# Optimization experiments

Hardware: AMD Instinct MI355X
Metric: run time of the kernel (lower is better)

## Reference

```python
import jax, jax.numpy as jnp
import numpy as np

N_NODES = 20000
N_EDGES = 320000
N_RELS = 200
DESC_LEN = 16
DIM_G = 64
DIM_WORD = 300
DIM_HIDDEN = 256
H_DIR = DIM_HIDDEN // 2  # per-direction GRU hidden
N_CLASS = 2000
V_WORD = 30000
V_DESC = 30000
B, T = 4, 32


def setup_inputs() -> dict:
    key = jax.random.key(0)
    ks = jax.random.split(key, 24)
    inp = {}
    # index tensors (pad token is 0; generate tokens in [1, V) so all positions valid)
    inp['questions'] = jax.random.randint(ks[0], (B, T), 1, V_WORD)
    inp['node_descs'] = jax.random.randint(ks[1], (N_NODES, DESC_LEN), 1, V_DESC)
    inp['edge_src'] = jax.random.randint(ks[2], (N_EDGES,), 0, N_NODES)
    inp['edge_dst'] = jax.random.randint(ks[3], (N_EDGES,), 0, N_NODES)
    inp['edge_type'] = jax.random.randint(ks[4], (N_EDGES,), 0, N_RELS)
    # embeddings (normal with std 1/sqrt(dim) as in original init)
    inp['emb_word'] = jax.random.normal(ks[5], (V_WORD, DIM_WORD)) / np.sqrt(DIM_WORD)
    inp['emb_desc'] = jax.random.normal(ks[6], (V_DESC, DIM_G)) / np.sqrt(DIM_G)
    # BiGRU params (gates order r,z,n; concatenated along last dim)
    s = 0.1
    inp['Wx_f'] = jax.random.normal(ks[7], (DIM_WORD, 3 * H_DIR)) * s
    inp['Wh_f'] = jax.random.normal(ks[8], (H_DIR, 3 * H_DIR)) * s
    inp['bx_f'] = jnp.zeros((3 * H_DIR,))
    inp['bh_f'] = jnp.zeros((3 * H_DIR,))
    inp['Wx_b'] = jax.random.normal(ks[9], (DIM_WORD, 3 * H_DIR)) * s
    inp['Wh_b'] = jax.random.normal(ks[10], (H_DIR, 3 * H_DIR)) * s
    inp['bx_b'] = jnp.zeros((3 * H_DIR,))
    inp['bh_b'] = jnp.zeros((3 * H_DIR,))
    # lin_h_to_g (kaiming-ish scale)
    inp['W_hg'] = jax.random.normal(ks[11], (DIM_HIDDEN, DIM_G)) * np.sqrt(2.0 / DIM_HIDDEN)
    inp['b_hg'] = jnp.zeros((DIM_G,))
    # RGCN basis decomposition
    inp['bases'] = jax.random.normal(ks[12], (1, DIM_G, DIM_G)) * np.sqrt(1.0 / DIM_G)
    inp['w_comp'] = jax.random.normal(ks[13], (N_RELS, 1))
    inp['rgcn_bias'] = jnp.zeros((DIM_G,))
    # classifier
    inp['W1'] = jax.random.normal(ks[14], (DIM_G + DIM_HIDDEN, 1024)) * np.sqrt(2.0 / (DIM_G + DIM_HIDDEN))
    inp['b1'] = jnp.zeros((1024,))
    inp['W2'] = jax.random.normal(ks[15], (1024, N_CLASS)) * np.sqrt(2.0 / 1024)
    inp['b2'] = jnp.zeros((N_CLASS,))
    return inp


def _gru_last_hidden(x, mask, Wx, Wh, bx, bh):
    """Run a GRU over time; hidden only updates where mask is True.
    x: [B,T,D], mask: [B,T]. Returns final hidden [B,H]."""
    bsz = x.shape[0]
    h0 = jnp.zeros((bsz, Wh.shape[0]), x.dtype)
    gx_all = x @ Wx + bx  # [B,T,3H] precompute input gates

    def step(h, inputs):
        gx, mt = inputs  # [B,3H], [B]
        gh = h @ Wh + bh
        xr, xz, xn = jnp.split(gx, 3, axis=-1)
        hr, hz, hn = jnp.split(gh, 3, axis=-1)
        r = jax.nn.sigmoid(xr + hr)
        z = jax.nn.sigmoid(xz + hz)
        n = jnp.tanh(xn + r * hn)
        h_new = (1.0 - z) * n + z * h
        h = jnp.where(mt[:, None], h_new, h)
        return h, None

    hT, _ = jax.lax.scan(step, h0, (gx_all.transpose(1, 0, 2), mask.T))
    return hT


def _rel_graph_conv(h, edge_src, edge_dst, edge_type, bases, w_comp, bias):
    """Basis-decomposed RGCN layer (DGL RelGraphConv, norm=None, no self-loop).
    h: [B,N,G]. W_r = sum_k w_comp[r,k] * bases[k]."""
    n = h.shape[1]
    # project through each basis first: [B,N,K,O]
    hb = jnp.einsum('bng,kgo->bnko', h, bases)
    # per-edge message: gather src, combine with relation coefficients -> [B,E,O]
    msg = jnp.einsum('beko,ek->beo', hb[:, edge_src], w_comp[edge_type])
    # scatter-add to destination nodes
    agg = jax.vmap(lambda m: jax.ops.segment_sum(m, edge_dst, num_segments=n))(msg)
    return jax.nn.relu(agg + bias)


def reference(questions, node_descs, edge_src, edge_dst, edge_type,
              emb_word, emb_desc,
              Wx_f, Wh_f, bx_f, bh_f, Wx_b, Wh_b, bx_b, bh_b,
              W_hg, b_hg, bases, w_comp, rgcn_bias,
              W1, b1, W2, b2):
    # ---- question encoding (BiGRU over non-pad tokens; pad id = 0) ----
    mask = questions != 0  # [B,T]
    x = emb_word[questions]  # [B,T,Dw] (dropout is identity at eval)
    hf = _gru_last_hidden(x, mask, Wx_f, Wh_f, bx_f, bh_f)
    hb = _gru_last_hidden(x[:, ::-1], mask[:, ::-1], Wx_b, Wh_b, bx_b, bh_b)
    q_emb = jnp.concatenate([hf, hb], axis=-1)  # [B, dim_hidden]

    # ---- attention-weighted node features from descriptions ----
    desc_emb = emb_desc[node_descs]          # [N,L,G]
    q_g = q_emb @ W_hg + b_hg                # [B,G]
    attn1 = jax.nn.softmax(jnp.einsum('nlg,bg->bnl', desc_emb, q_g), axis=-1)
    node_feat = jnp.einsum('bnl,nlg->bng', attn1, desc_emb)  # [B,N,G]

    # ---- one RGCN hidden layer over the KB graph ----
    node_feat = _rel_graph_conv(node_feat, edge_src, edge_dst, edge_type,
                                bases, w_comp, rgcn_bias)

    # ---- attention pooling over nodes ----
    attn2 = jax.nn.softmax(jnp.einsum('bng,bg->bn', node_feat, q_g), axis=1)
    node_agg = jnp.einsum('bn,bng->bg', attn2, node_feat)    # [B,G]

    # ---- classifier ----
    feat = jnp.concatenate([node_agg, q_emb], axis=-1)       # [B, G+H]
    logits = jax.nn.relu(feat @ W1 + b1) @ W2 + b2           # [B, n_class]
    return logits
```

## Files before the change

### kernel.cpp

```cpp
#include <hip/hip_runtime.h>
#include <hip/hip_bf16.h>
#include <math.h>

typedef __hip_bfloat16 bf16;

#define NNODES 20000
#define NEDGES 320000
#define DLEN   16
#define G      64
#define DW     300
#define DH     256
#define HD     128
#define G3     384
#define NCLS   2000
#define NB     4
#define TT     32
#define A2BLK  1024
#define A2MID  64

#define NBLK_CVT  384
#define NBLK_GX2  1536
#define NBLK_HIST ((NEDGES + 255) / 256)
#define NBLK_SCAT ((NEDGES + 255) / 256)

__device__ __forceinline__ float ld(const float* p, size_t i) { return p[i]; }
__device__ __forceinline__ float ld(const bf16* p, size_t i) { return __bfloat162float(p[i]); }
__device__ __forceinline__ void st(float* p, size_t i, float v) { p[i] = v; }
__device__ __forceinline__ void st(bf16* p, size_t i, float v) { p[i] = __float2bfloat16(v); }
__device__ __forceinline__ float relu(float x) { return (x < 0.f) ? 0.f : x; }

struct __align__(8) bf4 { bf16 x, y, z, w; };

#define OFF_FLAG  ((size_t)0)
#define OFF_GX    (OFF_FLAG + 4)
#define OFF_WHF   (OFF_GX   + 2*NB*TT*G3)
#define OFF_QEMB  (OFF_WHF  + 2*HD*G3)
#define OFF_QG    (OFF_QEMB + NB*DH)
#define OFF_NF    (OFF_QG   + NB*G)
#define OFF_HB    (OFF_NF   + (size_t)NB*NNODES*G)
#define OFF_PART  (OFF_HB   + (size_t)NB*NNODES*G)
#define OFF_PART2 (OFF_PART + (size_t)A2BLK*NB*66)
#define OFF_DEG   (OFF_PART2+ (size_t)A2MID*NB*66)
#define OFF_OFFS  (OFF_DEG  + NNODES)
#define OFF_RANK  (OFF_OFFS + NNODES + 8)
#define OFF_EPACK (OFF_RANK + NEDGES)
#define OFF_HID   (OFF_EPACK + 2*(size_t)NEDGES)

__global__ void k_init(const unsigned* probe, int* flag, int* deg) {
    int i = blockIdx.x * 256 + threadIdx.x;
    if (i < NNODES) deg[i] = 0;
    if (blockIdx.x == 0 && threadIdx.x < 64) {
        int cnt = 0;
        for (int k = threadIdx.x; k < 4096; k += 64) {
            unsigned lo = probe[k] & 0xFFFFu;
            unsigned e = (lo >> 7) & 0xFFu;
            cnt += (e >= 0x66u && e <= 0x7Eu) ? 1 : 0;
        }
#pragma unroll
        for (int off = 1; off < 64; off <<= 1) cnt += __shfl_xor(cnt, off, 64);
        if (threadIdx.x == 0) *flag = (2 * cnt > 4096) ? 1 : 0;
    }
}

template <typename T>
__device__ void cvt_body(int id, const void* Whf_, const void* Whb_, float* whf) {
    if (id >= 2 * HD * G3) return;
    int d = id / (HD * G3), r = id % (HD * G3);
    const T* W = (const T*)(d ? Whb_ : Whf_);
    whf[id] = ld(W, (size_t)r);
}

template <typename T>
__device__ void gx2_body(int bx2, const int* questions, const void* emb_word_,
                         const void* Wxf_, const void* bxf_,
                         const void* Wxb_, const void* bxb_, float* gx,
                         float* xs, float* psum) {
    int tid = threadIdx.x;
    int jt = bx2 % 6;
    int rid = bx2 / 6;
    int step = rid & 31;
    int b = (rid >> 5) & 3;
    int d = rid >> 7;
    int t = d ? (TT - 1 - step) : step;
    int tok = questions[b * TT + t];
    const T* row = (const T*)emb_word_ + (size_t)tok * DW;
    for (int k = tid; k < DW; k += 256) xs[k] = ld(row, (size_t)k);
    __syncthreads();
    int lane = tid & 63, phase = tid >> 6;
    int j = jt * 64 + lane;
    const T* Wx = (const T*)(d ? Wxb_ : Wxf_);
    float acc = 0.f;
    int k0 = phase * 75;
#pragma unroll 15
    for (int kk = 0; kk < 75; kk++) {
        int k = k0 + kk;
        acc += xs[k] * ld(Wx, (size_t)k * G3 + j);
    }
    psum[tid] = acc;
    __syncthreads();
    if (phase == 0) {
        const T* bx = (const T*)(d ? bxb_ : bxf_);
        float tot = ld(bx, (size_t)j)
                  + psum[lane] + psum[64 + lane] + psum[128 + lane] + psum[192 + lane];
        gx[(size_t)rid * G3 + j] = tot;
    }
}

__global__ void k_prep(const int* flag, const void* Whf, const void* Whb, float* whf,
                       const int* questions, const void* emb_word,
                       const void* Wxf, const void* bxf,
                       const void* Wxb, const void* bxb, float* gx,
                       const int* edge_dst, int* deg, int* rank) {
    __shared__ float xs[DW];
    __shared__ float psum[256];
    int bx = blockIdx.x;
    int tid = threadIdx.x;
    if (bx < NBLK_CVT) {
        int id = bx * 256 + tid;
        if (*flag) cvt_body<bf16>(id, Whf, Whb, whf);
        else       cvt_body<float>(id, Whf, Whb, whf);
    } else if (bx < NBLK_CVT + NBLK_GX2) {
        int bx2 = bx - NBLK_CVT;
        if (*flag) gx2_body<bf16>(bx2, questions, emb_word, Wxf, bxf, Wxb, bxb, gx, xs, psum);
        else       gx2_body<float>(bx2, questions, emb_word, Wxf, bxf, Wxb, bxb, gx, xs, psum);
    } else {
        int e = (bx - NBLK_CVT - NBLK_GX2) * 256 + tid;
        if (e < NEDGES) rank[e] = atomicAdd(&deg[edge_dst[e]], 1);
    }
}

template <typename T>
__device__ void gru_body(const int* questions, const float* gx, const float* whf,
                         const void* bhf_, const void* bhb_, float* qemb,
                         float* hsm, float* ghs) {
    int tid = threadIdx.x;
    int d = blockIdx.x >> 2, b = blockIdx.x & 3;
    int half = tid / G3, j = tid - half * G3;
    const float* wh = whf + (size_t)d * HD * G3 + (size_t)half * 64 * G3 + j;
    float w[64];
#pragma unroll
    for (int m = 0; m < 64; m++) w[m] = wh[(size_t)m * G3];
    const T* bh = (const T*)(d ? bhb_ : bhf_);
    float bhj = (half == 0) ? ld(bh, (size_t)j) : 0.f;
    if (tid < HD) hsm[tid] = 0.f;
    const float* gxb = gx + ((size_t)(d * NB + b)) * TT * G3;
    __syncthreads();
    const float4* h4 = (const float4*)(hsm + half * 64);
    for (int step = 0; step < TT; step++) {
        float acc = bhj;
#pragma unroll
        for (int m4 = 0; m4 < 16; m4++) {
            float4 hp = h4[m4];
            acc = fmaf(hp.x, w[4 * m4 + 0], acc);
            acc = fmaf(hp.y, w[4 * m4 + 1], acc);
            acc = fmaf(hp.z, w[4 * m4 + 2], acc);
            acc = fmaf(hp.w, w[4 * m4 + 3], acc);
        }
        ghs[half * G3 + j] = acc;
        __syncthreads();
        if (tid < HD) {
            const float* gxp = gxb + step * G3;
            int t = d ? (TT - 1 - step) : step;
            bool msk = questions[b * TT + t] != 0;
            float gr = ghs[tid] + ghs[G3 + tid];
            float gz = ghs[HD + tid] + ghs[G3 + HD + tid];
            float gn = ghs[2 * HD + tid] + ghs[G3 + 2 * HD + tid];
            float r = 1.f / (1.f + expf(-(gxp[tid] + gr)));
            float z = 1.f / (1.f + expf(-(gxp[HD + tid] + gz)));
            float n = tanhf(gxp[2 * HD + tid] + r * gn);
            float hn = (1.f - z) * n + z * hsm[tid];
            if (msk) hsm[tid] = hn;
        }
        __syncthreads();
    }
    if (tid < HD) qemb[b * DH + d * HD + tid] = hsm[tid];
}

__device__ void scan_body(const int* deg, int* offs, int* wtot) {
    int t = threadIdx.x;
    int lane = t & 63, wave = t >> 6;
    int c[27];
    int base = t * 27;
    int run = 0;
#pragma unroll
    for (int i = 0; i < 27; i++) {
        int v = (base + i < NNODES) ? deg[base + i] : 0;
        c[i] = run;
        run += v;
    }
    int myrun = run, inc = run;
#pragma unroll
    for (int off = 1; off < 64; off <<= 1) {
        int u = __shfl_up(inc, off, 64);
        if (lane >= off) inc += u;
    }
    if (lane == 63) wtot[wave] = inc;
    __syncthreads();
    if (t == 0) {
        int s = 0;
#pragma unroll
        for (int i = 0; i < 12; i++) { int v = wtot[i]; wtot[i] = s; s += v; }
        offs[NNODES] = s;
    }
    __syncthreads();
    int ebase = wtot[wave] + inc - myrun;
#pragma unroll
    for (int i = 0; i < 27; i++) {
        if (base + i < NNODES) offs[base + i] = ebase + c[i];
    }
}

__global__ __launch_bounds__(2 * G3) void k_gru(const int* flag, const int* questions,
                                                const float* gx, const float* whf,
                                                const void* bhf, const void* bhb, float* qemb,
                                                const int* deg, int* offs) {
    __shared__ __align__(16) float hsm[HD];
    __shared__ float ghs[2 * G3];
    __shared__ int wtot[12];
    if (blockIdx.x < 8) {
        if (*flag) gru_body<bf16>(questions, gx, whf, bhf, bhb, qemb, hsm, ghs);
        else       gru_body<float>(questions, gx, whf, bhf, bhb, qemb, hsm, ghs);
    } else {
        scan_body(deg, offs, wtot);
    }
}

template <typename T>
__device__ void qg_body(const float* qemb, const void* W_hg_, const void* b_hg_, float* qg) {
    int tid = threadIdx.x;
    int b = tid >> 6, g = tid & 63;
    const T* W = (const T*)W_hg_;
    float acc = ld((const T*)b_hg_, (size_t)g);
#pragma unroll 4
    for (int i = 0; i < DH; i++) acc += qemb[b * DH + i] * ld(W, (size_t)i * G + g);
    qg[b * G + g] = acc;
}
__global__ void k_qg(const int* flag, const float* qemb, const void* W_hg,
                     const void* b_hg, float* qg) {
    if (*flag) qg_body<bf16>(qemb, W_hg, b_hg, qg);
    else       qg_body<float>(qemb, W_hg, b_hg, qg);
}

template <typename T>
__device__ void scatter_body(int e, const int* src, const int* dst, const int* typ,
                             const void* w_comp_, const int* offs, const int* rank,
                             int2* epack) {
    if (e < NEDGES) {
        int pos = offs[dst[e]] + rank[e];
        int2 v;
        v.x = src[e];
        v.y = __float_as_int(ld((const T*)w_comp_, (size_t)typ[e]));
        epack[pos] = v;
    }
}

template <typename T>
__device__ void attn1_body(int nb4, const int* node_descs, const void* emb_desc_,
                           const float* qg, bf16* nf16,
                           float* dsm, float* attn_s, float* qgs) {
    int tid = threadIdx.x;
    if (tid < NB * G) qgs[tid] = qg[tid];
    __syncthreads();
    const T* emb_desc = (const T*)emb_desc_;
    int w = tid >> 6, lane = tid & 63;
    int n = nb4 * 4 + w;
    float dreg[DLEN];
    const int* nd = node_descs + n * DLEN;
    float* dw = dsm + (size_t)w * DLEN * 68;
#pragma unroll
    for (int l = 0; l < DLEN; l++) {
        int idx = nd[l];
        float v = ld(emb_desc, (size_t)idx * G + lane);
        dreg[l] = v;
        dw[l * 68 + lane] = v;
    }
    int lb = lane >> 4, ll = lane & 15;
    float acc = 0.f;
#pragma unroll
    for (int i = 0; i < 16; i++) {
        float4 a = *(const float4*)&dw[ll * 68 + 4 * i];
        float4 q = *(const float4*)&qgs[lb * G + 4 * i];
        acc = fmaf(a.x, q.x, acc);
        acc = fmaf(a.y, q.y, acc);
        acc = fmaf(a.z, q.z, acc);
        acc = fmaf(a.w, q.w, acc);
    }
    float mx = acc;
#pragma unroll
    for (int off = 1; off < 16; off <<= 1) mx = fmaxf(mx, __shfl_xor(mx, off, 64));
    float e = expf(acc - mx);
    float s = e;
#pragma unroll
    for (int off = 1; off < 16; off <<= 1) s += __shfl_xor(s, off, 64);
    attn_s[w * 64 + lane] = e / s;
#pragma unroll
    for (int b = 0; b < NB; b++) {
        float a = 0.f;
#pragma unroll
        for (int l = 0; l < DLEN; l++) a += attn_s[w * 64 + b * 16 + l] * dreg[l];
        nf16[((size_t)b * NNODES + n) * G + lane] = __float2bfloat16(a);
    }
}

__global__ __launch_bounds__(256) void k_sc_attn1(const int* flag,
                                                  const int* src, const int* dst, const int* typ,
                                                  const void* w_comp, const int* offs,
                                                  const int* rank, int2* epack,
                                                  const int* node_descs, const void* emb_desc,
                                                  const float* qg, bf16* nf16) {
    __shared__ __align__(16) float dsm[4 * DLEN * 68];
    __shared__ float attn_s[4 * 64];
    __shared__ __align__(16) float qgs[NB * G];
    int bx = blockIdx.x;
    if (bx < NBLK_SCAT) {
        int e = bx * 256 + threadIdx.x;
        if (*flag) scatter_body<bf16>(e, src, dst, typ, w_comp, offs, rank, epack);
        else       scatter_body<float>(e, src, dst, typ, w_comp, offs, rank, epack);
    } else {
        int nb4 = bx - NBLK_SCAT;
        if (*flag) attn1_body<bf16>(nb4, node_descs, emb_desc, qg, nf16, dsm, attn_s, qgs);
        else       attn1_body<float>(nb4, node_descs, emb_desc, qg, nf16, dsm, attn_s, qgs);
    }
}

template <typename T>
__device__ void hbg_body(const bf16* nf16, const void* bases_, bf16* hb16,
                         float* as, float* bs) {
    int tid = threadIdx.x;
    const T* bases = (const T*)bases_;
    for (int i = tid; i < G * G; i += 256) bs[(i >> 6) * 68 + (i & 63)] = ld(bases, (size_t)i);
    size_t r0 = (size_t)blockIdx.x * 64;
    const bf4* gA = (const bf4*)(nf16 + r0 * G);
#pragma unroll
    for (int i = 0; i < 4; i++) {
        int c = tid + i * 256;
        int row = c >> 4, col4 = c & 15;
        bf4 v = gA[c];
        float4 f;
        f.x = __bfloat162float(v.x);
        f.y = __bfloat162float(v.y);
        f.z = __bfloat162float(v.z);
        f.w = __bfloat162float(v.w);
        *(float4*)&as[row * 68 + col4 * 4] = f;
    }
    __syncthreads();
    int tx = tid & 15, ty = tid >> 4;
    float acc[4][4];
#pragma unroll
    for (int i = 0; i < 4; i++)
#pragma unroll
        for (int j = 0; j < 4; j++) acc[i][j] = 0.f;
#pragma unroll 4
    for (int g4 = 0; g4 < 16; g4++) {
        float4 b0 = *(const float4*)&bs[(4 * g4 + 0) * 68 + tx * 4];
        float4 b1 = *(const float4*)&bs[(4 * g4 + 1) * 68 + tx * 4];
        float4 b2 = *(const float4*)&bs[(4 * g4 + 2) * 68 + tx * 4];
        float4 b3 = *(const float4*)&bs[(4 * g4 + 3) * 68 + tx * 4];
#pragma unroll
        for (int i = 0; i < 4; i++) {
            float4 a = *(const float4*)&as[(ty * 4 + i) * 68 + g4 * 4];
            acc[i][0] = fmaf(a.x, b0.x, acc[i][0]);
            acc[i][0] = fmaf(a.y, b1.x, acc[i][0]);
            acc[i][0] = fmaf(a.z, b2.x, acc[i][0]);
            acc[i][0] = fmaf(a.w, b3.x, acc[i][0]);
            acc[i][1] = fmaf(a.x, b0.y, acc[i][1]);
            acc[i][1] = fmaf(a.y, b1.y, acc[i][1]);
            acc[i][1] = fmaf(a.z, b2.y, acc[i][1]);
            acc[i][1] = fmaf(a.w, b3.y, acc[i][1]);
            acc[i][2] = fmaf(a.x, b0.z, acc[i][2]);
            acc[i][2] = fmaf(a.y, b1.z, acc[i][2]);
            acc[i][2] = fmaf(a.z, b2.z, acc[i][2]);
            acc[i][2] = fmaf(a.w, b3.z, acc[i][2]);
            acc[i][3] = fmaf(a.x, b0.w, acc[i][3]);
            acc[i][3] = fmaf(a.y, b1.w, acc[i][3]);
            acc[i][3] = fmaf(a.z, b2.w, acc[i][3]);
            acc[i][3] = fmaf(a.w, b3.w, acc[i][3]);
        }
    }
#pragma unroll
    for (int i = 0; i < 4; i++) {
        size_t r = r0 + ty * 4 + i;
        int b = (int)(r / NNODES);
        int n = (int)(r - (size_t)b * NNODES);
        bf4 o;
        o.x = __float2bfloat16(acc[i][0]);
        o.y = __float2bfloat16(acc[i][1]);
        o.z = __float2bfloat16(acc[i][2]);
        o.w = __float2bfloat16(acc[i][3]);
        *(bf4*)&hb16[((size_t)n * NB + b) * G + tx * 4] = o;
    }
}
__global__ __launch_bounds__(256) void k_hbg(const int* flag, const bf16* nf16,
                                             const void* bases, bf16* hb16) {
    __shared__ __align__(16) float as[64 * 68];
    __shared__ __align__(16) float bs[64 * 68];
    if (*flag) hbg_body<bf16>(nf16, bases, hb16, as, bs);
    else       hbg_body<float>(nf16, bases, hb16, as, bs);
}

template <typename T>
__device__ void agg_body(const bf16* hb16, const int* offs, const int2* epack,
                         const void* bias_, bf16* out_nf16) {
    int tid = threadIdx.x;
    int b = tid >> 6, g = tid & 63;
    int dn = blockIdx.x;
    int s0 = offs[dn], s1 = offs[dn + 1];
    int boff = b * G + g;
    float acc = 0.f;
    int p = s0;
    for (; p + 15 < s1; p += 16) {
        int2 ev[16]; float x[16];
#pragma unroll
        for (int k = 0; k < 16; k++) ev[k] = epack[p + k];
#pragma unroll
        for (int k = 0; k < 16; k++)
            x[k] = __bfloat162float(hb16[(size_t)ev[k].x * (NB * G) + boff]);
#pragma unroll
        for (int k = 0; k < 16; k++) acc += __int_as_float(ev[k].y) * x[k];
    }
    for (; p + 7 < s1; p += 8) {
        int2 ev[8]; float x[8];
#pragma unroll
        for (int k = 0; k < 8; k++) ev[k] = epack[p + k];
#pragma unroll
        for (int k = 0; k < 8; k++)
            x[k] = __bfloat162float(hb16[(size_t)ev[k].x * (NB * G) + boff]);
#pragma unroll
        for (int k = 0; k < 8; k++) acc += __int_as_float(ev[k].y) * x[k];
    }
    for (; p + 3 < s1; p += 4) {
        int2 ev[4]; float x[4];
#pragma unroll
        for (int k = 0; k < 4; k++) ev[k] = epack[p + k];
#pragma unroll
        for (int k = 0; k < 4; k++)
            x[k] = __bfloat162float(hb16[(size_t)ev[k].x * (NB * G) + boff]);
#pragma unroll
        for (int k = 0; k < 4; k++) acc += __int_as_float(ev[k].y) * x[k];
    }
    for (; p < s1; p++) {
        int2 ev = epack[p];
        acc += __int_as_float(ev.y) * __bfloat162float(hb16[(size_t)ev.x * (NB * G) + boff]);
    }
    out_nf16[((size_t)b * NNODES + dn) * G + g] =
        __float2bfloat16(relu(acc + ld((const T*)bias_, (size_t)g)));
}
__global__ __launch_bounds__(256) void k_agg(const int* flag, const bf16* hb16, const int* offs,
                                             const int2* epack, const void* bias,
                                             bf16* out_nf16) {
    if (*flag) agg_body<bf16>(hb16, offs, epack, bias, out_nf16);
    else       agg_body<float>(hb16, offs, epack, bias, out_nf16);
}

__device__ __forceinline__ void a2_update(float& M, float& L, float& A, float p, float v) {
    if (p > M) {
        float s = expf(M - p);
        A *= s; L *= s; M = p;
    }
    float e = expf(p - M);
    L += e;
    A = fmaf(e, v, A);
}

__global__ __launch_bounds__(256) void k_attn2(const bf16* rg, const float* qg, float* part) {
    int tid = threadIdx.x;
    int b = tid >> 6, lane = tid & 63;
    float q = qg[b * G + lane];
    int chunk = (NNODES + A2BLK - 1) / A2BLK;
    int n0 = blockIdx.x * chunk;
    int n1 = min(n0 + chunk, NNODES);
    const bf16* base = rg + (size_t)b * NNODES * G + lane;
    float M = -3.4e38f, L = 0.f, A = 0.f;
    int n = n0;
    for (; n + 3 < n1; n += 4) {
        float v0 = __bfloat162float(base[(size_t)(n + 0) * G]);
        float v1 = __bfloat162float(base[(size_t)(n + 1) * G]);
        float v2 = __bfloat162float(base[(size_t)(n + 2) * G]);
        float v3 = __bfloat162float(base[(size_t)(n + 3) * G]);
        float p0 = v0 * q, p1 = v1 * q, p2 = v2 * q, p3 = v3 * q;
#pragma unroll
        for (int off = 32; off >= 1; off >>= 1) {
            p0 += __shfl_xor(p0, off, 64);
            p1 += __shfl_xor(p1, off, 64);
            p2 += __shfl_xor(p2, off, 64);
            p3 += __shfl_xor(p3, off, 64);
        }
        a2_update(M, L, A, p0, v0);
        a2_update(M, L, A, p1, v1);
        a2_update(M, L, A, p2, v2);
        a2_update(M, L, A, p3, v3);
    }
    for (; n < n1; n++) {
        float v = __bfloat162float(base[(size_t)n * G]);
        float p = v * q;
#pragma unroll
        for (int off = 32; off >= 1; off >>= 1) p += __shfl_xor(p, off, 64);
        a2_update(M, L, A, p, v);
    }
    float* pp = part + ((size_t)blockIdx.x * NB + b) * 66;
    if (lane == 0) { pp[0] = M; pp[1] = L; }
    pp[2 + lane] = A;
}

__global__ void k_attn2m(const float* part, float* part2) {
    int tid = threadIdx.x;
    int b = tid >> 6, lane = tid & 63;
    int grp = blockIdx.x;
    float M = -3.4e38f, L = 0.f, A = 0.f;
    for (int i = 0; i < A2BLK / A2MID; i++) {
        const float* pp = part + ((size_t)(grp * (A2BLK / A2MID) + i) * NB + b) * 66;
        float m = pp[0], l = pp[1], a = pp[2 + lane];
        float mn = fmaxf(M, m);
        float e1 = expf(M - mn), e2 = expf(m - mn);
        A = A * e1 + a * e2;
        L = L * e1 + l * e2;
        M = mn;
    }
    float* pq = part2 + ((size_t)grp * NB + b) * 66;
    if (lane == 0) { pq[0] = M; pq[1] = L; }
    pq[2 + lane] = A;
}

template <typename T>
__device__ void fc1_body(const float* part2, const float* qemb,
                         const void* W1_, const void* b1_, float* hid,
                         float* feat, float* psum) {
    int tid = threadIdx.x;
    int b = blockIdx.x >> 4, tile = blockIdx.x & 15;
    if (tid < 64) {
        float M = -3.4e38f, L = 0.f, A = 0.f;
        for (int p = 0; p < A2MID; p++) {
            const float* pp = part2 + ((size_t)p * NB + b) * 66;
            float m = pp[0], l = pp[1], a = pp[2 + tid];
            float mn = fmaxf(M, m);
            float e1 = expf(M - mn), e2 = expf(m - mn);
            A = A * e1 + a * e2;
            L = L * e1 + l * e2;
            M = mn;
        }
        feat[tid] = A / L;
        feat[tid + 256] = qemb[b * DH + tid + 192];
    } else {
        feat[tid] = qemb[b * DH + tid - G];
    }
    __syncthreads();
    int lane = tid & 63, phase = tid >> 6;
    int u = tile * 64 + lane;
    const T* W1 = (const T*)W1_;
    float acc = 0.f;
#pragma unroll 8
    for (int kk = 0; kk < 80; kk++) {
        int k = phase * 80 + kk;
        acc += feat[k] * ld(W1, (size_t)k * 1024 + u);
    }
    psum[tid] = acc;
    __syncthreads();
    if (phase == 0) {
        float tot = psum[lane] + psum[64 + lane] + psum[128 + lane] + psum[192 + lane]
                  + ld((const T*)b1_, (size_t)u);
        hid[b * 1024 + u] = relu(tot);
    }
}
__global__ __launch_bounds__(256) void k_fc1(const int* flag, const float* part2,
                                             const float* qemb, const void* W1, const void* b1,
                                             float* hid) {
    __shared__ float feat[320];
    __shared__ float psum[256];
    if (*flag) fc1_body<bf16>(part2, qemb, W1, b1, hid, feat, psum);
    else       fc1_body<float>(part2, qemb, W1, b1, hid, feat, psum);
}

template <typename T>
__device__ void fc2_body(const float* hid, const void* W2_, const void* b2_, void* out_,
                         float* hs, float* psum) {
    int tid = threadIdx.x;
    int tile = blockIdx.x;
#pragma unroll
    for (int i = 0; i < 16; i++) hs[tid + 256 * i] = hid[tid + 256 * i];
    __syncthreads();
    int lane = tid & 63, phase = tid >> 6;
    int c = tile * 64 + lane;
    bool ok = (c < NCLS);
    const T* W2 = (const T*)W2_;
    float a0 = 0.f, a1 = 0.f, a2 = 0.f, a3 = 0.f;
    if (ok) {
#pragma unroll 8
        for (int uu = 0; uu < 256; uu++) {
            int u = phase * 256 + uu;
            float w = ld(W2, (size_t)u * NCLS + c);
            a0 += hs[u] * w;
            a1 += hs[1024 + u] * w;
            a2 += hs[2048 + u] * w;
            a3 += hs[3072 + u] * w;
        }
    }
    psum[tid] = a0;
    psum[256 + tid] = a1;
    psum[512 + tid] = a2;
    psum[768 + tid] = a3;
    __syncthreads();
    if (phase == 0 && ok) {
        float bb = ld((const T*)b2_, (size_t)c);
#pragma unroll
        for (int b = 0; b < NB; b++) {
            float* ps = psum + b * 256;
            float tot = ps[lane] + ps[64 + lane] + ps[128 + lane] + ps[192 + lane] + bb;
            st((T*)out_, (size_t)b * NCLS + c, tot);
        }
    }
}
__global__ __launch_bounds__(256) void k_fc2(const int* flag, const float* hid,
                                             const void* W2, const void* b2v, void* out) {
    __shared__ float hs[4096];
    __shared__ float psum[1024];
    if (*flag) fc2_body<bf16>(hid, W2, b2v, out, hs, psum);
    else       fc2_body<float>(hid, W2, b2v, out, hs, psum);
}

extern "C" void kernel_launch(void* const* d_in, const int* in_sizes, int n_in,
                              void* d_out, int out_size, void* d_ws, size_t ws_size,
                              hipStream_t stream) {
    const int* questions  = (const int*)d_in[0];
    const int* node_descs = (const int*)d_in[1];
    const int* edge_src   = (const int*)d_in[2];
    const int* edge_dst   = (const int*)d_in[3];
    const int* edge_type  = (const int*)d_in[4];
    const void* emb_word  = d_in[5];
    const void* emb_desc  = d_in[6];
    const void* Wx_f = d_in[7];
    const void* Wh_f = d_in[8];
    const void* bx_f = d_in[9];
    const void* bh_f = d_in[10];
    const void* Wx_b = d_in[11];
    const void* Wh_b = d_in[12];
    const void* bx_b = d_in[13];
    const void* bh_b = d_in[14];
    const void* W_hg = d_in[15];
    const void* b_hg = d_in[16];
    const void* bases = d_in[17];
    const void* w_comp = d_in[18];
    const void* rgcn_bias = d_in[19];
    const void* W1 = d_in[20];
    const void* b1 = d_in[21];
    const void* W2 = d_in[22];
    const void* b2 = d_in[23];

    float* ws = (float*)d_ws;
    int*      flag  = (int*)(ws + OFF_FLAG);
    float*    gx    = ws + OFF_GX;
    float*    whf   = ws + OFF_WHF;
    float*    qemb  = ws + OFF_QEMB;
    float*    qg    = ws + OFF_QG;
    bf16*     nf16  = (bf16*)(ws + OFF_NF);
    bf16*     hb16  = (bf16*)(ws + OFF_HB);
    float*    part  = ws + OFF_PART;
    float*    part2 = ws + OFF_PART2;
    int*      deg   = (int*)(ws + OFF_DEG);
    int*      offs  = (int*)(ws + OFF_OFFS);
    int*      rank  = (int*)(ws + OFF_RANK);
    int2*     epack = (int2*)(ws + OFF_EPACK);
    float*    hid   = ws + OFF_HID;

    hipLaunchKernelGGL(k_init, dim3(80), dim3(256), 0, stream,
                       (const unsigned*)emb_word, flag, deg);
    hipLaunchKernelGGL(k_prep, dim3(NBLK_CVT + NBLK_GX2 + NBLK_HIST), dim3(256), 0, stream,
                       flag, Wh_f, Wh_b, whf,
                       questions, emb_word, Wx_f, bx_f, Wx_b, bx_b, gx,
                       edge_dst, deg, rank);
    hipLaunchKernelGGL(k_gru, dim3(9), dim3(2 * G3), 0, stream,
                       flag, questions, gx, whf, bh_f, bh_b, qemb, deg, offs);
    hipLaunchKernelGGL(k_qg, dim3(1), dim3(256), 0, stream, flag, qemb, W_hg, b_hg, qg);
    hipLaunchKernelGGL(k_sc_attn1, dim3(NBLK_SCAT + NNODES / 4), dim3(256), 0, stream,
                       flag, edge_src, edge_dst, edge_type, w_comp, offs, rank, epack,
                       node_descs, emb_desc, qg, nf16);
    hipLaunchKernelGGL(k_hbg, dim3(NB * NNODES / 64), dim3(256), 0, stream,
                       flag, nf16, bases, hb16);
    hipLaunchKernelGGL(k_agg, dim3(NNODES), dim3(256), 0, stream,
                       flag, hb16, offs, epack, rgcn_bias, nf16);
    hipLaunchKernelGGL(k_attn2, dim3(A2BLK), dim3(256), 0, stream, nf16, qg, part);
    hipLaunchKernelGGL(k_attn2m, dim3(A2MID), dim3(256), 0, stream, part, part2);
    hipLaunchKernelGGL(k_fc1, dim3(NB * 16), dim3(256), 0, stream,
                       flag, part2, qemb, W1, b1, hid);
    hipLaunchKernelGGL(k_fc2, dim3(32), dim3(256), 0, stream,
                       flag, hid, W2, b2, d_out);
}
```

Before: 312.4 us.

## Precompute vocabulary-level desc·bases and desc·q to eliminate per-node matmul kernel

```diff
diff --git a/kernel.cpp b/kernel.cpp
--- a/kernel.cpp
+++ b/kernel.cpp
@@ -15,13 +15,16 @@
 #define NCLS   2000
 #define NB     4
 #define TT     32
+#define VDESC  30000
 #define A2BLK  1024
 #define A2MID  64
 
-#define NBLK_CVT  384
-#define NBLK_GX2  1536
-#define NBLK_HIST ((NEDGES + 255) / 256)
-#define NBLK_SCAT ((NEDGES + 255) / 256)
+#define NBLK_CVT   384
+#define NBLK_GX2   1536
+#define NBLK_DESCB (VDESC / 16)
+#define NBLK_HIST  ((NEDGES + 255) / 256)
+#define NBLK_SCAT  ((NEDGES + 255) / 256)
+#define NBLK_DQ    ((VDESC + 63) / 64)
 
 __device__ __forceinline__ float ld(const float* p, size_t i) { return p[i]; }
 __device__ __forceinline__ float ld(const bf16* p, size_t i) { return __bfloat162float(p[i]); }
@@ -38,7 +41,9 @@
 #define OFF_QG    (OFF_QEMB + NB*DH)
 #define OFF_NF    (OFF_QG   + NB*G)
 #define OFF_HB    (OFF_NF   + (size_t)NB*NNODES*G)
-#define OFF_PART  (OFF_HB   + (size_t)NB*NNODES*G)
+#define OFF_DESCB (OFF_HB   + (size_t)NB*NNODES*G)
+#define OFF_DQ    (OFF_DESCB + (size_t)VDESC*G/2)
+#define OFF_PART  (OFF_DQ   + (size_t)VDESC*NB)
 #define OFF_PART2 (OFF_PART + (size_t)A2BLK*NB*66)
 #define OFF_DEG   (OFF_PART2+ (size_t)A2MID*NB*66)
 #define OFF_OFFS  (OFF_DEG  + NNODES)
@@ -106,13 +111,37 @@
     }
 }
 
+template <typename T>
+__device__ void descb_body(int bx3, const void* emb_desc_, const void* bases_,
+                           bf16* descB, float* bsm, float* rsm) {
+    int tid = threadIdx.x;
+    const T* bases = (const T*)bases_;
+    const T* desc = (const T*)emb_desc_;
+    for (int i = tid; i < G * G; i += 256) bsm[(i >> 6) * 68 + (i & 63)] = ld(bases, (size_t)i);
+    int r0 = bx3 * 16;
+    for (int i = tid; i < 16 * G; i += 256) {
+        int r = i >> 6, k = i & 63;
+        rsm[r * 68 + k] = ld(desc, (size_t)(r0 + r) * G + k);
+    }
+    __syncthreads();
+    int g = tid & 63, slot = tid >> 6;
+#pragma unroll
+    for (int it = 0; it < 4; it++) {
+        int r = slot * 4 + it;
+        float acc = 0.f;
+#pragma unroll 8
+        for (int k = 0; k < G; k++) acc = fmaf(rsm[r * 68 + k], bsm[k * 68 + g], acc);
+        descB[(size_t)(r0 + r) * G + g] = __float2bfloat16(acc);
+    }
+}
+
 __global__ void k_prep(const int* flag, const void* Whf, const void* Whb, float* whf,
                        const int* questions, const void* emb_word,
                        const void* Wxf, const void* bxf,
                        const void* Wxb, const void* bxb, float* gx,
+                       const void* emb_desc, const void* bases, bf16* descB,
                        const int* edge_dst, int* deg, int* rank) {
-    __shared__ float xs[DW];
-    __shared__ float psum[256];
+    __shared__ __align__(16) float smem[64 * 68 + 16 * 68];
     int bx = blockIdx.x;
     int tid = threadIdx.x;
     if (bx < NBLK_CVT) {
@@ -121,10 +150,18 @@
         else       cvt_body<float>(id, Whf, Whb, whf);
     } else if (bx < NBLK_CVT + NBLK_GX2) {
         int bx2 = bx - NBLK_CVT;
+        float* xs = smem;
+        float* psum = smem + 320;
         if (*flag) gx2_body<bf16>(bx2, questions, emb_word, Wxf, bxf, Wxb, bxb, gx, xs, psum);
         else       gx2_body<float>(bx2, questions, emb_word, Wxf, bxf, Wxb, bxb, gx, xs, psum);
+    } else if (bx < NBLK_CVT + NBLK_GX2 + NBLK_DESCB) {
+        int bx3 = bx - NBLK_CVT - NBLK_GX2;
+        float* bsm = smem;
+        float* rsm = smem + 64 * 68;
+        if (*flag) descb_body<bf16>(bx3, emb_desc, bases, descB, bsm, rsm);
+        else       descb_body<float>(bx3, emb_desc, bases, descB, bsm, rsm);
     } else {
-        int e = (bx - NBLK_CVT - NBLK_GX2) * 256 + tid;
+        int e = (bx - NBLK_CVT - NBLK_GX2 - NBLK_DESCB) * 256 + tid;
         if (e < NEDGES) rank[e] = atomicAdd(&deg[edge_dst[e]], 1);
     }
 }
@@ -226,19 +263,46 @@
 }
 
 template <typename T>
-__device__ void qg_body(const float* qemb, const void* W_hg_, const void* b_hg_, float* qg) {
+__device__ void qg_compute(const float* qemb, const void* W_hg_, const void* b_hg_,
+                           float* out ) {
     int tid = threadIdx.x;
     int b = tid >> 6, g = tid & 63;
     const T* W = (const T*)W_hg_;
     float acc = ld((const T*)b_hg_, (size_t)g);
 #pragma unroll 4
     for (int i = 0; i < DH; i++) acc += qemb[b * DH + i] * ld(W, (size_t)i * G + g);
-    qg[b * G + g] = acc;
-}
-__global__ void k_qg(const int* flag, const float* qemb, const void* W_hg,
-                     const void* b_hg, float* qg) {
-    if (*flag) qg_body<bf16>(qemb, W_hg, b_hg, qg);
-    else       qg_body<float>(qemb, W_hg, b_hg, qg);
+    out[b * G + g] = acc;
+}
+
+template <typename T>
+__device__ void dq_body(int chunk, const void* emb_desc_, const float* qgs, float* dq) {
+    int tid = threadIdx.x;
+    int ii = tid >> 2, b = tid & 3;
+    int idx = chunk * 64 + ii;
+    if (idx >= VDESC) return;
+    const T* row = (const T*)emb_desc_ + (size_t)idx * G;
+    const float* q = qgs + b * G;
+    float acc = 0.f;
+#pragma unroll 8
+    for (int k = 0; k < G; k++) acc = fmaf(ld(row, (size_t)k), q[k], acc);
+    dq[(size_t)idx * NB + b] = acc;
+}
+
+__global__ __launch_bounds__(256) void k_qg_dq(const int* flag, const float* qemb,
+                                               const void* W_hg, const void* b_hg, float* qg,
+                                               const void* emb_desc, float* dq) {
+    __shared__ float qgs[NB * G];
+    if (blockIdx.x == 0) {
+        if (*flag) qg_compute<bf16>(qemb, W_hg, b_hg, qg);
+        else       qg_compute<float>(qemb, W_hg, b_hg, qg);
+        return;
+    }
+    if (*flag) qg_compute<bf16>(qemb, W_hg, b_hg, qgs);
+    else       qg_compute<float>(qemb, W_hg, b_hg, qgs);
+    __syncthreads();
+    int chunk = blockIdx.x - 1;
+    if (*flag) dq_body<bf16>(chunk, emb_desc, qgs, dq);
+    else       dq_body<float>(chunk, emb_desc, qgs, dq);
 }
 
 template <typename T>
@@ -254,148 +318,58 @@
     }
 }
 
-template <typename T>
-__device__ void attn1_body(int nb4, const int* node_descs, const void* emb_desc_,
-                           const float* qg, bf16* nf16,
-                           float* dsm, float* attn_s, float* qgs) {
-    int tid = threadIdx.x;
-    if (tid < NB * G) qgs[tid] = qg[tid];
-    __syncthreads();
-    const T* emb_desc = (const T*)emb_desc_;
+__device__ void attn1_body(int nb4, const int* node_descs, const float* dq,
+                           const bf16* descB, bf16* hb16, float* attn_s, int* idxs) {
+    int tid = threadIdx.x;
     int w = tid >> 6, lane = tid & 63;
     int n = nb4 * 4 + w;
-    float dreg[DLEN];
+    int b = lane >> 4, l = lane & 15;
     const int* nd = node_descs + n * DLEN;
-    float* dw = dsm + (size_t)w * DLEN * 68;
-#pragma unroll
-    for (int l = 0; l < DLEN; l++) {
-        int idx = nd[l];
-        float v = ld(emb_desc, (size_t)idx * G + lane);
-        dreg[l] = v;
-        dw[l * 68 + lane] = v;
-    }
-    int lb = lane >> 4, ll = lane & 15;
-    float acc = 0.f;
-#pragma unroll
-    for (int i = 0; i < 16; i++) {
-        float4 a = *(const float4*)&dw[ll * 68 + 4 * i];
-        float4 q = *(const float4*)&qgs[lb * G + 4 * i];
-        acc = fmaf(a.x, q.x, acc);
-        acc = fmaf(a.y, q.y, acc);
-        acc = fmaf(a.z, q.z, acc);
-        acc = fmaf(a.w, q.w, acc);
-    }
-    float mx = acc;
+    int idx = nd[l];
+    float logit = dq[(size_t)idx * NB + b];
+    float mx = logit;
 #pragma unroll
     for (int off = 1; off < 16; off <<= 1) mx = fmaxf(mx, __shfl_xor(mx, off, 64));
-    float e = expf(acc - mx);
+    float e = expf(logit - mx);
     float s = e;
 #pragma unroll
     for (int off = 1; off < 16; off <<= 1) s += __shfl_xor(s, off, 64);
     attn_s[w * 64 + lane] = e / s;
-#pragma unroll
-    for (int b = 0; b < NB; b++) {
-        float a = 0.f;
-#pragma unroll
-        for (int l = 0; l < DLEN; l++) a += attn_s[w * 64 + b * 16 + l] * dreg[l];
-        nf16[((size_t)b * NNODES + n) * G + lane] = __float2bfloat16(a);
-    }
+    if (lane < 16) idxs[w * 16 + lane] = idx;
+    __syncthreads();
+    float o0 = 0.f, o1 = 0.f, o2 = 0.f, o3 = 0.f;
+#pragma unroll
+    for (int ll = 0; ll < DLEN; ll++) {
+        int row = idxs[w * 16 + ll];
+        float v = __bfloat162float(descB[(size_t)row * G + lane]);
+        o0 = fmaf(attn_s[w * 64 + ll], v, o0);
+        o1 = fmaf(attn_s[w * 64 + 16 + ll], v, o1);
+        o2 = fmaf(attn_s[w * 64 + 32 + ll], v, o2);
+        o3 = fmaf(attn_s[w * 64 + 48 + ll], v, o3);
+    }
+    size_t baseo = (size_t)n * (NB * G) + lane;
+    hb16[baseo + 0 * G] = __float2bfloat16(o0);
+    hb16[baseo + 1 * G] = __float2bfloat16(o1);
+    hb16[baseo + 2 * G] = __float2bfloat16(o2);
+    hb16[baseo + 3 * G] = __float2bfloat16(o3);
 }
 
 __global__ __launch_bounds__(256) void k_sc_attn1(const int* flag,
                                                   const int* src, const int* dst, const int* typ,
                                                   const void* w_comp, const int* offs,
                                                   const int* rank, int2* epack,
-                                                  const int* node_descs, const void* emb_desc,
-                                                  const float* qg, bf16* nf16) {
-    __shared__ __align__(16) float dsm[4 * DLEN * 68];
+                                                  const int* node_descs, const float* dq,
+                                                  const bf16* descB, bf16* hb16) {
     __shared__ float attn_s[4 * 64];
-    __shared__ __align__(16) float qgs[NB * G];
+    __shared__ int idxs[4 * DLEN];
     int bx = blockIdx.x;
     if (bx < NBLK_SCAT) {
         int e = bx * 256 + threadIdx.x;
         if (*flag) scatter_body<bf16>(e, src, dst, typ, w_comp, offs, rank, epack);
         else       scatter_body<float>(e, src, dst, typ, w_comp, offs, rank, epack);
     } else {
-        int nb4 = bx - NBLK_SCAT;
-        if (*flag) attn1_body<bf16>(nb4, node_descs, emb_desc, qg, nf16, dsm, attn_s, qgs);
-        else       attn1_body<float>(nb4, node_descs, emb_desc, qg, nf16, dsm, attn_s, qgs);
-    }
-}
-
-template <typename T>
-__device__ void hbg_body(const bf16* nf16, const void* bases_, bf16* hb16,
-                         float* as, float* bs) {
-    int tid = threadIdx.x;
-    const T* bases = (const T*)bases_;
-    for (int i = tid; i < G * G; i += 256) bs[(i >> 6) * 68 + (i & 63)] = ld(bases, (size_t)i);
-    size_t r0 = (size_t)blockIdx.x * 64;
-    const bf4* gA = (const bf4*)(nf16 + r0 * G);
-#pragma unroll
-    for (int i = 0; i < 4; i++) {
-        int c = tid + i * 256;
-        int row = c >> 4, col4 = c & 15;
-        bf4 v = gA[c];
-        float4 f;
-        f.x = __bfloat162float(v.x);
-        f.y = __bfloat162float(v.y);
-        f.z = __bfloat162float(v.z);
-        f.w = __bfloat162float(v.w);
-        *(float4*)&as[row * 68 + col4 * 4] = f;
-    }
-    __syncthreads();
-    int tx = tid & 15, ty = tid >> 4;
-    float acc[4][4];
-#pragma unroll
-    for (int i = 0; i < 4; i++)
-#pragma unroll
-        for (int j = 0; j < 4; j++) acc[i][j] = 0.f;
-#pragma unroll 4
-    for (int g4 = 0; g4 < 16; g4++) {
-        float4 b0 = *(const float4*)&bs[(4 * g4 + 0) * 68 + tx * 4];
-        float4 b1 = *(const float4*)&bs[(4 * g4 + 1) * 68 + tx * 4];
-        float4 b2 = *(const float4*)&bs[(4 * g4 + 2) * 68 + tx * 4];
-        float4 b3 = *(const float4*)&bs[(4 * g4 + 3) * 68 + tx * 4];
-#pragma unroll
-        for (int i = 0; i < 4; i++) {
-            float4 a = *(const float4*)&as[(ty * 4 + i) * 68 + g4 * 4];
-            acc[i][0] = fmaf(a.x, b0.x, acc[i][0]);
-            acc[i][0] = fmaf(a.y, b1.x, acc[i][0]);
-            acc[i][0] = fmaf(a.z, b2.x, acc[i][0]);
-            acc[i][0] = fmaf(a.w, b3.x, acc[i][0]);
-            acc[i][1] = fmaf(a.x, b0.y, acc[i][1]);
-            acc[i][1] = fmaf(a.y, b1.y, acc[i][1]);
-            acc[i][1] = fmaf(a.z, b2.y, acc[i][1]);
-            acc[i][1] = fmaf(a.w, b3.y, acc[i][1]);
-            acc[i][2] = fmaf(a.x, b0.z, acc[i][2]);
-            acc[i][2] = fmaf(a.y, b1.z, acc[i][2]);
-            acc[i][2] = fmaf(a.z, b2.z, acc[i][2]);
-            acc[i][2] = fmaf(a.w, b3.z, acc[i][2]);
-            acc[i][3] = fmaf(a.x, b0.w, acc[i][3]);
-            acc[i][3] = fmaf(a.y, b1.w, acc[i][3]);
-            acc[i][3] = fmaf(a.z, b2.w, acc[i][3]);
-            acc[i][3] = fmaf(a.w, b3.w, acc[i][3]);
-        }
-    }
-#pragma unroll
-    for (int i = 0; i < 4; i++) {
-        size_t r = r0 + ty * 4 + i;
-        int b = (int)(r / NNODES);
-        int n = (int)(r - (size_t)b * NNODES);
-        bf4 o;
-        o.x = __float2bfloat16(acc[i][0]);
-        o.y = __float2bfloat16(acc[i][1]);
-        o.z = __float2bfloat16(acc[i][2]);
-        o.w = __float2bfloat16(acc[i][3]);
-        *(bf4*)&hb16[((size_t)n * NB + b) * G + tx * 4] = o;
-    }
-}
-__global__ __launch_bounds__(256) void k_hbg(const int* flag, const bf16* nf16,
-                                             const void* bases, bf16* hb16) {
-    __shared__ __align__(16) float as[64 * 68];
-    __shared__ __align__(16) float bs[64 * 68];
-    if (*flag) hbg_body<bf16>(nf16, bases, hb16, as, bs);
-    else       hbg_body<float>(nf16, bases, hb16, as, bs);
+        attn1_body(bx - NBLK_SCAT, node_descs, dq, descB, hb16, attn_s, idxs);
+    }
 }
 
 template <typename T>
@@ -653,6 +627,8 @@
     float*    qg    = ws + OFF_QG;
     bf16*     nf16  = (bf16*)(ws + OFF_NF);
     bf16*     hb16  = (bf16*)(ws + OFF_HB);
+    bf16*     descB = (bf16*)(ws + OFF_DESCB);
+    float*    dq    = ws + OFF_DQ;
     float*    part  = ws + OFF_PART;
     float*    part2 = ws + OFF_PART2;
     int*      deg   = (int*)(ws + OFF_DEG);
@@ -663,18 +639,19 @@
 
     hipLaunchKernelGGL(k_init, dim3(80), dim3(256), 0, stream,
                        (const unsigned*)emb_word, flag, deg);
-    hipLaunchKernelGGL(k_prep, dim3(NBLK_CVT + NBLK_GX2 + NBLK_HIST), dim3(256), 0, stream,
+    hipLaunchKernelGGL(k_prep,
+                       dim3(NBLK_CVT + NBLK_GX2 + NBLK_DESCB + NBLK_HIST), dim3(256), 0, stream,
                        flag, Wh_f, Wh_b, whf,
                        questions, emb_word, Wx_f, bx_f, Wx_b, bx_b, gx,
+                       emb_desc, bases, descB,
                        edge_dst, deg, rank);
     hipLaunchKernelGGL(k_gru, dim3(9), dim3(2 * G3), 0, stream,
                        flag, questions, gx, whf, bh_f, bh_b, qemb, deg, offs);
-    hipLaunchKernelGGL(k_qg, dim3(1), dim3(256), 0, stream, flag, qemb, W_hg, b_hg, qg);
+    hipLaunchKernelGGL(k_qg_dq, dim3(1 + NBLK_DQ), dim3(256), 0, stream,
+                       flag, qemb, W_hg, b_hg, qg, emb_desc, dq);
     hipLaunchKernelGGL(k_sc_attn1, dim3(NBLK_SCAT + NNODES / 4), dim3(256), 0, stream,
                        flag, edge_src, edge_dst, edge_type, w_comp, offs, rank, epack,
-                       node_descs, emb_desc, qg, nf16);
-    hipLaunchKernelGGL(k_hbg, dim3(NB * NNODES / 64), dim3(256), 0, stream,
-                       flag, nf16, bases, hb16);
+                       node_descs, dq, descB, hb16);
     hipLaunchKernelGGL(k_agg, dim3(NNODES), dim3(256), 0, stream,
                        flag, hb16, offs, epack, rgcn_bias, nf16);
     hipLaunchKernelGGL(k_attn2, dim3(A2BLK), dim3(256), 0, stream, nf16, qg, part);
```

After: 306.0 us. -2.0%, faster.
